# Kernel optimization log

Measured on AMD Instinct MI355X. Metric: run time of the kernel, lower is better.

The kernel has to match this reference:

```python
import jax, jax.numpy as jnp
import numpy as np
from jax import lax

H_IMG, W_IMG = 1280, 1280
STRIDES = (8, 16, 32, 64, 128)
FEAT_SHAPES = tuple((H_IMG // s) * (W_IMG // s) for s in STRIDES)  # (25600,6400,1600,400,100)
N_POINTS = sum(FEAT_SHAPES)  # 34100
NUM_CLASSES = 1
TOPK = 1000
SCORE_THRESH = 0.05
NMS_THRESH = 0.5
MAX_DET = 300
BATCH = 8
N_GT = 200


def make_points():
    # matches AnchorFreePS.reference_points: cell centers at stride*i + stride//2, (cx, cy) order
    pts = []
    for s in STRIDES:
        h, w = H_IMG // s, W_IMG // s
        cx = np.arange(w, dtype=np.float32) * s + s // 2
        cy = np.arange(h, dtype=np.float32) * s + s // 2
        gy, gx = np.meshgrid(cy, cx, indexing='ij')
        pts.append(np.stack([gx, gy], axis=-1).reshape(-1, 2))
    return jnp.asarray(np.concatenate(pts, axis=0))


def setup_inputs() -> dict:
    key = jax.random.key(0)
    k1, k2, k3, k4 = jax.random.split(key, 4)
    points = make_points()  # [N,2]
    xy = jax.random.uniform(k1, (BATCH, N_GT, 2), minval=0.0, maxval=1000.0)
    wh = jax.random.uniform(k2, (BATCH, N_GT, 2), minval=20.0, maxval=260.0)
    gt_boxes = jnp.concatenate([xy, xy + wh], axis=-1)  # [B,M,4] x1y1x2y2
    cls_logits = jax.random.normal(k3, (BATCH, N_POINTS, NUM_CLASSES)) * 1.5 - 3.0
    regression = jax.random.uniform(k4, (BATCH, N_POINTS, 4)) * 0.1  # normalized ltrb codes
    return {"points": points, "gt_boxes": gt_boxes, "cls_logits": cls_logits, "regression": regression}


def match_points_to_boxes(points, gt_boxes):
    # point-in-box test + area-cost argmin (compute_loss matched_idxs)
    px = points[None, :, None, 0]  # [1,N,1]
    py = points[None, :, None, 1]
    b = gt_boxes[:, None, :, :]    # [B,1,M,4]
    inside = (px >= b[..., 0]) & (px <= b[..., 2]) & (py >= b[..., 1]) & (py <= b[..., 3])  # [B,N,M]
    matched = jnp.any(inside, axis=-1)  # [B,N]
    areas = (gt_boxes[..., 2] - gt_boxes[..., 0]) * (gt_boxes[..., 3] - gt_boxes[..., 1])  # [B,M]
    BIG = jnp.float32(2 ** 31 - 1)  # torch.iinfo(torch.int).max
    cost = jnp.where(inside, areas[:, None, :], BIG)
    idx = jnp.argmin(cost, axis=-1)
    return jnp.where(matched, idx, -1)


def decode_boxes(rel, pts):
    # FCOSBoxCoder.decode_single with weights (1,1,1,1)
    l = rel[:, 0] * W_IMG
    t = rel[:, 1] * H_IMG
    r = rel[:, 2] * W_IMG
    b = rel[:, 3] * H_IMG
    x, y = pts[:, 0], pts[:, 1]
    return jnp.stack([x - l, y - t, x + r, y + b], axis=-1)


def clip_boxes(boxes):
    return jnp.stack([
        jnp.clip(boxes[:, 0], 0.0, W_IMG),
        jnp.clip(boxes[:, 1], 0.0, H_IMG),
        jnp.clip(boxes[:, 2], 0.0, W_IMG),
        jnp.clip(boxes[:, 3], 0.0, H_IMG)], axis=-1)


def nms(boxes, scores, labels, valid_init):
    # fixed-size sequential NMS equivalent to batched_nms (same-label suppression)
    work = lax.stop_gradient(jnp.where(valid_init, scores, -jnp.inf))

    def body(w, _):
        i = jnp.argmax(w)
        s = w[i]
        box = boxes[i]
        x1 = jnp.maximum(box[0], boxes[:, 0])
        y1 = jnp.maximum(box[1], boxes[:, 1])
        x2 = jnp.minimum(box[2], boxes[:, 2])
        y2 = jnp.minimum(box[3], boxes[:, 3])
        inter = jnp.clip(x2 - x1, 0.0) * jnp.clip(y2 - y1, 0.0)
        a1 = (box[2] - box[0]) * (box[3] - box[1])
        a2 = (boxes[:, 2] - boxes[:, 0]) * (boxes[:, 3] - boxes[:, 1])
        iou = inter / (a1 + a2 - inter + 1e-9)
        supp = (iou > NMS_THRESH) & (labels == labels[i])
        w = jnp.where(supp, -jnp.inf, w).at[i].set(-jnp.inf)
        return w, (i, s)

    _, (idxs, picked) = lax.scan(body, work, None, length=MAX_DET)
    valid = picked > -jnp.inf
    return idxs, valid


def postprocess_image(points, cls_i, reg_i):
    bx_list, sc_list, lb_list = [], [], []
    off = 0
    for size in FEAT_SHAPES:  # fixed small level loop
        sl = slice(off, off + size)
        off += size
        scores = jax.nn.sigmoid(cls_i[sl]).reshape(-1)  # [size*C]
        k = min(TOPK, size * NUM_CLASSES)
        sc, idx = lax.top_k(scores, k)
        a = idx // NUM_CLASSES
        lb = idx % NUM_CLASSES
        bx = clip_boxes(decode_boxes(reg_i[sl][a], points[sl][a]))
        bx_list.append(bx)
        sc_list.append(sc)
        lb_list.append(lb)
    boxes = jnp.concatenate(bx_list, axis=0)
    scores = jnp.concatenate(sc_list, axis=0)
    labels = jnp.concatenate(lb_list, axis=0)
    idxs, valid = nms(boxes, scores, labels, scores > SCORE_THRESH)
    out_boxes = jnp.where(valid[:, None], boxes[idxs], 0.0)
    out_scores = jnp.where(valid, scores[idxs], 0.0)
    out_labels = jnp.where(valid, labels[idxs], -1)
    return out_boxes, out_scores, out_labels, valid


def reference(points, gt_boxes, cls_logits, regression):
    matched_idxs = match_points_to_boxes(points, gt_boxes)  # [B,N]
    boxes, scores, labels, valid = jax.vmap(
        lambda c, r: postprocess_image(points, c, r))(cls_logits, regression)
    return matched_idxs, boxes, scores, labels, valid
```

## Files before the change

### kernel.cpp

```cpp
#include <hip/hip_runtime.h>
#include <stdint.h>

#define N_POINTS   34100
#define BATCH      8
#define N_GT       200
#define NLEV       5
#define NCAND      3500
#define MAX_DET    300
#define SCORE_TH   0.05f
#define NMS_TH     0.5f
#define IMG        1280.0f
#define NBIN       4096
#define TIE_CAP    4096
#define MTH 0.50000002980232238769531250

#define OUT_MATCH  0
#define OUT_BOXES  272800
#define OUT_SCORES 282400
#define OUT_LABELS 284800
#define OUT_VALID  287200

#define WS_KEYS    0
#define WS_SBOX    2632192
#define WS_SSC     3080192
#define WS_MASK    3192192
#define WS_DIAG    9500032
#define WS_HIST    WS_MASK
#define HSUB       8
#define MASK_STRIDE 98560
#define DIAG_STRIDE 3520


typedef unsigned long long u64;
typedef uint32_t u32;

__device__ __forceinline__ int mask_off(int c) {
    int g = c >> 6;
    return 64 * (55 * g - (g * (g - 1)) / 2) + (c - (g << 6)) * (55 - g);
}

__device__ __forceinline__ int level_of(int p) {
    return (p < 25600) ? 0 : (p < 32000) ? 1 : (p < 33600) ? 2 : (p < 34000) ? 3 : 4;
}
__device__ __forceinline__ int loff_of(int l) {
    return (l == 0) ? 0 : (l == 1) ? 25600 : (l == 2) ? 32000 : (l == 3) ? 33600 : 34000;
}
__device__ __forceinline__ int k_of(int l) {
    return (l == 0) ? 1000 : (l == 1) ? 1000 : (l == 2) ? 1000 : (l == 3) ? 400 : 100;
}
__device__ __forceinline__ u64 readlane64(u64 v, int t) {
    u32 lo = (u32)__builtin_amdgcn_readlane((int)(u32)v, t);
    u32 hi = (u32)__builtin_amdgcn_readlane((int)(u32)(v >> 32), t);
    return ((u64)hi << 32) | lo;
}

__global__ __launch_bounds__(1024)
void match_hist_kernel(const float* __restrict__ points,
                       const float* __restrict__ gt,
                       const float* __restrict__ logits,
                       float* __restrict__ out_match,
                       u32* __restrict__ keys,
                       u32* __restrict__ ghist) {
#pragma clang fp contract(off)
    __shared__ float bx1[N_GT], by1[N_GT], bx2[N_GT], by2[N_GT], ar[N_GT];
    __shared__ u32 hh[NBIN];
    const int b = blockIdx.x & 7;
    const int g = blockIdx.x >> 3;
    const int tid = threadIdx.x;

    if (g < 17) {
        const int base = g * 2048 + tid;
        for (int j = tid; j < N_GT; j += 1024) {
            float x1 = gt[(b * N_GT + j) * 4 + 0];
            float y1 = gt[(b * N_GT + j) * 4 + 1];
            float x2 = gt[(b * N_GT + j) * 4 + 2];
            float y2 = gt[(b * N_GT + j) * 4 + 3];
            bx1[j] = x1; by1[j] = y1; bx2[j] = x2; by2[j] = y2;
            ar[j] = (x2 - x1) * (y2 - y1);
        }
        __syncthreads();

        const float BIGF = 2147483648.0f;
        float px[2], py[2], best[2];
        int bi[2];
#pragma unroll
        for (int k = 0; k < 2; ++k) {
            int p = base + k * 1024;
            int pc = (p < N_POINTS) ? p : 0;
            px[k] = points[pc * 2 + 0];
            py[k] = points[pc * 2 + 1];
            best[k] = BIGF; bi[k] = -1;
        }
        for (int j = 0; j < N_GT; ++j) {
            float x1 = bx1[j], y1 = by1[j], x2 = bx2[j], y2 = by2[j], a = ar[j];
#pragma unroll
            for (int k = 0; k < 2; ++k) {
                bool inside = (px[k] >= x1) && (px[k] <= x2) &&
                              (py[k] >= y1) && (py[k] <= y2);
                float cost = inside ? a : BIGF;
                if (cost < best[k]) { best[k] = cost; bi[k] = j; }
            }
        }
#pragma unroll
        for (int k = 0; k < 2; ++k) {
            int p = base + k * 1024;
            if (p >= N_POINTS) continue;
            out_match[b * N_POINTS + p] = (float)bi[k];
        }
    } else {
        const int f = g - 17;
        int lev, sub, p0, cnt;
        if (f < 8)       { lev = 0; sub = f;     p0 = f * 3200;               cnt = 3200; }
        else if (f < 10) { lev = 1; sub = f - 8; p0 = 25600 + (f - 8) * 3200; cnt = 3200; }
        else if (f == 10){ lev = 2; sub = 0;     p0 = 32000;                  cnt = 1600; }
        else if (f == 11){ lev = 3; sub = 0;     p0 = 33600;                  cnt = 400;  }
        else             { lev = 4; sub = 0;     p0 = 34000;                  cnt = 100;  }

        for (int i = tid; i < NBIN; i += 1024) hh[i] = 0u;
        __syncthreads();

        for (int i = tid; i < cnt; i += 1024) {
            int p = p0 + i;
            float lg = logits[b * N_POINTS + p];
            float s = 1.0f / (1.0f + expf(-lg));
            u32 u = __float_as_uint(s);
            u32 key = (u & 0x80000000u) ? ~u : (u | 0x80000000u);
            keys[b * N_POINTS + p] = key;
            atomicAdd(&hh[(key >> 19) & 4095u], 1u);
        }
        __syncthreads();

        u32* outp = ghist + (((u32)b * NLEV + (u32)lev) * HSUB + (u32)sub) * NBIN;
        for (int i = tid; i < NBIN; i += 1024) outp[i] = hh[i];
    }
}

#define SORT_T 1024
#define LSWZ(j) (((j) & 63) * 65 + ((j) >> 6))
__global__ __launch_bounds__(SORT_T)
void pipeline_kernel(const u32* __restrict__ keys,
                     const u32* __restrict__ ghist,
                     const float* __restrict__ reg,
                     const float* __restrict__ points,
                     float* __restrict__ sboxes,
                     float* __restrict__ sscores) {
#pragma clang fp contract(off)
    __shared__ __align__(16) char smem[131072];
    u64* sk   = (u64*)smem;
    u64* tb   = (u64*)(smem + 32768);
    u64* aux  = (u64*)(smem + 65536);
    u32* h    = (u32*)(smem + 98304);
    u32* bs   = (u32*)(smem + 114688);
    u32* lsb  = (u32*)smem;
    __shared__ u32 sTl[NLEV], skkl[NLEV], wt[16];
    __shared__ u32 scnt, stcnt;

    const int b = blockIdx.x;
    const int tid = threadIdx.x;
    const int lane = tid & 63;
    const int wid = tid >> 6;
    const u32* kk_ = keys + b * N_POINTS;

    if (tid == 0) { scnt = 0u; stcnt = 0u; }

    {
        const u32* hb = ghist + (u32)b * (NLEV * HSUB * NBIN);
#pragma unroll
        for (int lev = 0; lev < NLEV; ++lev) {
            const int SUBS = (lev == 0) ? 8 : (lev == 1) ? 2 : 1;
            const u32* hl = hb + lev * HSUB * NBIN + tid;
            u32 s0 = 0, s1 = 0, s2 = 0, s3 = 0;
#pragma unroll
            for (int sub = 0; sub < SUBS; ++sub) {
                const u32* hs = hl + sub * NBIN;
                s0 += hs[0]; s1 += hs[1024]; s2 += hs[2048]; s3 += hs[3072];
            }
            u32* lv = lsb + lev * 4160;
            lv[LSWZ(tid)]        = s0;
            lv[LSWZ(tid + 1024)] = s1;
            lv[LSWZ(tid + 2048)] = s2;
            lv[LSWZ(tid + 3072)] = s3;
        }
        const uint4* kp4 = (const uint4*)kk_;
        u32 a0 = 0, a1 = 0, a2 = 0, a3 = 0;
        int i = tid;
        for (; i + 3072 < 8525; i += 4096) {
            uint4 v0 = kp4[i];
            uint4 v1 = kp4[i + 1024];
            uint4 v2 = kp4[i + 2048];
            uint4 v3 = kp4[i + 3072];
            a0 ^= v0.x ^ v0.y ^ v0.z ^ v0.w;
            a1 ^= v1.x ^ v1.y ^ v1.z ^ v1.w;
            a2 ^= v2.x ^ v2.y ^ v2.z ^ v2.w;
            a3 ^= v3.x ^ v3.y ^ v3.z ^ v3.w;
        }
        for (; i < 8525; i += 1024) {
            uint4 v = kp4[i];
            a0 ^= v.x ^ v.y ^ v.z ^ v.w;
        }
        u32 wacc = a0 ^ a1 ^ a2 ^ a3;
        asm volatile("" :: "v"(wacc));
    }
    __syncthreads();

    if (wid < NLEV) {
        const u32 K = (u32)k_of(wid);
        const u32* hh = lsb + wid * 4160;
        u32 S = 0;
#pragma unroll 16
        for (int i = 0; i < 64; ++i) S += hh[i * 65 + lane];
        u32 acc = S;
#pragma unroll
        for (int off = 1; off < 64; off <<= 1) {
            u32 v = (u32)__shfl_down((int)acc, off);
            if (lane + off < 64) acc += v;
        }
        u32 sfxAfter = acc - S;
        bool hit = (sfxAfter < K) && (sfxAfter + S >= K);
        u64 bal = __ballot(hit);
        int Lg = (int)__builtin_ctzll(bal);
        u32 sfxG = (u32)__shfl((int)sfxAfter, Lg);

        u32 v = hh[lane * 65 + Lg];
        u32 acc2 = v;
#pragma unroll
        for (int off = 1; off < 64; off <<= 1) {
            u32 t = (u32)__shfl_down((int)acc2, off);
            if (lane + off < 64) acc2 += t;
        }
        u32 sfx2 = sfxG + acc2 - v;
        bool hit2 = (sfx2 < K) && (sfx2 + v >= K);
        if (hit2) { sTl[wid] = (u32)(Lg * 64 + lane); skkl[wid] = K - sfx2; }
    }
    __syncthreads();

    const u64 below = (lane == 0) ? 0ull : (~0ull >> (64 - lane));
    const int CHUNK = 4 * SORT_T;
    for (int it = 0; it < (N_POINTS + CHUNK - 1) / CHUNK; ++it) {
        u32 key4[4]; int pc4[4]; bool act4[4];
#pragma unroll
        for (int u = 0; u < 4; ++u) {
            int i = it * CHUNK + u * SORT_T + tid;
            act4[u] = (i < N_POINTS);
            pc4[u] = act4[u] ? i : (N_POINTS - 1);
            key4[u] = kk_[pc4[u]];
        }
#pragma unroll
        for (int u = 0; u < 4; ++u) {
            bool active = act4[u];
            int pc = pc4[u];
            u32 key = key4[u];
            int l = level_of(pc);
            u32 digit = (key >> 19) & 4095u;
            u32 T = sTl[l];
            bool isDef = active && (digit > T);
            bool isTie = active && (digit == T);
            u64 k50 = ((u64)key << 18) | ((u64)(7 - l) << 15)
                    | (u64)(32767 - (pc - loff_of(l)));
            u64 grp = __ballot(isDef);
            if (grp) {
                int leader = (int)__builtin_ctzll(grp);
                u32 base_ = 0;
                if (lane == leader)
                    base_ = atomicAdd(&scnt, (u32)__builtin_popcountll(grp));
                base_ = (u32)__shfl((int)base_, leader);
                if (isDef) sk[base_ + (u32)__builtin_popcountll(grp & below)] = k50;
            }
            u64 tg = __ballot(isTie);
            if (tg) {
                int leader = (int)__builtin_ctzll(tg);
                u32 base_ = 0;
                if (lane == leader)
                    base_ = atomicAdd(&stcnt, (u32)__builtin_popcountll(tg));
                base_ = (u32)__shfl((int)base_, leader);
                if (isTie) {
                    u32 pos = base_ + (u32)__builtin_popcountll(tg & below);
                    if (pos < TIE_CAP) tb[pos] = k50;
                }
            }
        }
    }
    __syncthreads();

    int t = (int)stcnt; if (t > TIE_CAP) t = TIE_CAP;
    for (int j0 = tid; j0 - tid < t; j0 += SORT_T) {
        bool active = j0 < t;
        u64 kj = active ? tb[j0] : 0ull;
        u32 lvtag = (u32)(kj >> 15) & 7u;
        int r = 0;
        for (int i = 0; i < t; ++i) {
            u64 ki = tb[i];
            r += (ki > kj && (((u32)(ki >> 15) & 7u) == lvtag)) ? 1 : 0;
        }
        bool inc = active && (r < (int)skkl[7 - lvtag]);
        u64 grp = __ballot(inc);
        if (grp) {
            int leader = (int)__builtin_ctzll(grp);
            u32 base_ = 0;
            if (lane == leader)
                base_ = atomicAdd(&scnt, (u32)__builtin_popcountll(grp));
            base_ = (u32)__shfl((int)base_, leader);
            if (inc) sk[base_ + (u32)__builtin_popcountll(grp & below)] = kj;
        }
    }
    __syncthreads();
    const int total = (int)scnt;

    for (int i = tid; i < NBIN; i += SORT_T) h[i] = 0u;
    __syncthreads();
    for (int i = tid; i < total; i += SORT_T)
        atomicAdd(&h[(u32)(sk[i] >> 37) & 4095u], 1u);
    __syncthreads();

    u32 t0 = h[4095 - 4 * tid];
    u32 t1 = h[4095 - (4 * tid + 1)];
    u32 t2 = h[4095 - (4 * tid + 2)];
    u32 t3 = h[4095 - (4 * tid + 3)];
    u32 tsum = t0 + t1 + t2 + t3;
    u32 sc_ = tsum;
#pragma unroll
    for (int off = 1; off < 64; off <<= 1) {
        u32 v = (u32)__shfl_up((int)sc_, off);
        if (lane >= off) sc_ += v;
    }
    if (lane == 63) wt[wid] = sc_;
    __syncthreads();
    if (tid < 64) {
        u32 v = (tid < 16) ? wt[tid] : 0u;
        u32 s2 = v;
#pragma unroll
        for (int off = 1; off < 16; off <<= 1) {
            u32 x = (u32)__shfl_up((int)s2, off);
            if (tid >= off) s2 += x;
        }
        if (tid < 16) wt[tid] = s2 - v;
    }
    __syncthreads();
    u32 run = (sc_ - tsum) + wt[wid];
    bs[4095 - 4 * tid] = run;       run += t0;
    bs[4095 - (4 * tid + 1)] = run; run += t1;
    bs[4095 - (4 * tid + 2)] = run; run += t2;
    bs[4095 - (4 * tid + 3)] = run;
    __syncthreads();
    for (int i = tid; i < NBIN; i += SORT_T) h[i] = 0u;
    __syncthreads();
    for (int i = tid; i < total; i += SORT_T) {
        u64 k = sk[i];
        u32 d = (u32)(k >> 37) & 4095u;
        u32 pos = bs[d] + atomicAdd(&h[d], 1u);
        aux[pos] = k;
    }
    __syncthreads();
    for (int p = tid; p < total; p += SORT_T) {
        u64 kp = aux[p];
        u32 d = (u32)(kp >> 37) & 4095u;
        u32 gbase = bs[d];
        u32 gend = (d == 0) ? (u32)total : bs[d - 1];
        u32 r = 0;
        for (u32 q = gbase; q < gend; ++q) r += (aux[q] > kp) ? 1u : 0u;
        sk[gbase + r] = kp;
    }
    __syncthreads();

    for (int r = tid; r < NCAND; r += SORT_T) {
        float x1 = 0.f, y1 = 0.f, x2 = 0.f, y2 = 0.f, sc = 0.f;
        if (r < total) {
            u64 k50 = sk[r];
            int lowb = (int)(k50 & 0x3FFFFull);
            int l = 7 - (lowb >> 15);
            int idxl = 32767 - (lowb & 32767);
            int p = loff_of(l) + idxl;
            u32 key32 = (u32)(k50 >> 18);
            sc = __uint_as_float(key32 ^ 0x80000000u);
            int gp = b * N_POINTS + p;
            float l_ = reg[gp * 4 + 0] * IMG;
            float t_ = reg[gp * 4 + 1] * IMG;
            float r_ = reg[gp * 4 + 2] * IMG;
            float bb = reg[gp * 4 + 3] * IMG;
            float px = points[p * 2 + 0];
            float py = points[p * 2 + 1];
            x1 = fminf(fmaxf(px - l_, 0.0f), IMG);
            y1 = fminf(fmaxf(py - t_, 0.0f), IMG);
            x2 = fminf(fmaxf(px + r_, 0.0f), IMG);
            y2 = fminf(fmaxf(py + bb, 0.0f), IMG);
        }
        int slot = b * NCAND + r;
        sboxes[slot * 4 + 0] = x1;
        sboxes[slot * 4 + 1] = y1;
        sboxes[slot * 4 + 2] = x2;
        sboxes[slot * 4 + 3] = y2;
        sscores[slot] = sc;
    }
}

__global__ __launch_bounds__(256)
void mask_kernel(const float* __restrict__ sboxes,
                 const float* __restrict__ sscores,
                 u64* __restrict__ mask,
                 u64* __restrict__ diag) {
#pragma clang fp contract(off)
    const int b = blockIdx.x & 7;
    const int gx = blockIdx.x >> 3;
    const int wv = threadIdx.x >> 6;
    const int lane = threadIdx.x & 63;
    const int NG = (NCAND + 3) >> 2;
    const int NH = (NG + 1) >> 1;
    const int gidx = gx * 4 + wv;
    if (gidx >= NH) return;

    const float4* gb = (const float4*)sboxes + b * NCAND;
    const float* gs = sscores + b * NCAND;
    u64* mout = mask + (size_t)b * MASK_STRIDE;
    u64* dout = diag + (size_t)b * DIAG_STRIDE;

    for (int s = 0; s < 2; ++s) {
        const int g0 = (s == 0) ? gidx : (NG - 1 - gidx);
        if (s == 1 && g0 == gidx) break;
        const int c0 = g0 << 2;

        float4 bc[4]; float a1[4]; bool ok[4]; int g[4]; u64* rp[4];
        bool any = false;
#pragma unroll
        for (int i = 0; i < 4; ++i) {
            int c = c0 + i;
            int cc = (c < NCAND) ? c : (NCAND - 1);
            bc[i] = gb[cc];
            a1[i] = (bc[i].z - bc[i].x) * (bc[i].w - bc[i].y);
            ok[i] = (c < NCAND) && (gs[cc] > SCORE_TH);
            g[i] = cc >> 6;
            rp[i] = mout + mask_off(cc) - g[i];
            any |= ok[i];
        }
        if (!any) continue;

        for (int w = (c0 >> 6); w < 55; ++w) {
            int cj = (w << 6) + lane;
            float4 bj = (cj < NCAND) ? gb[cj] : make_float4(0.f, 0.f, 0.f, 0.f);
            float a2 = (bj.z - bj.x) * (bj.w - bj.y);
#pragma unroll
            for (int i = 0; i < 4; ++i) {
                float x1 = fmaxf(bc[i].x, bj.x);
                float y1 = fmaxf(bc[i].y, bj.y);
                float x2 = fminf(bc[i].z, bj.z);
                float y2 = fminf(bc[i].w, bj.w);
                float inter = fmaxf(x2 - x1, 0.f) * fmaxf(y2 - y1, 0.f);
                float denom = a1[i] + a2 - inter + 1e-9f;
                float hf = 0.5f * denom;
                float rr = fmaf(0x1p-25f, denom, hf);
                u64 bits = __ballot(inter > rr);
                u64 eq = __ballot(inter == rr);
                if (eq) {
                    u64 fb = __ballot((double)inter > MTH * (double)denom);
                    bits |= (eq & fb);
                }
                if (lane == 0 && ok[i] && w >= g[i]) {
                    rp[i][w] = bits;
                    if (w == g[i]) dout[c0 + i] = bits;
                }
            }
        }
    }
}

__global__ __launch_bounds__(1024)
void scan_kernel(const float* __restrict__ sboxes,
                 const float* __restrict__ sscores,
                 const u64* __restrict__ mask,
                 const u64* __restrict__ diag,
                 float* __restrict__ out) {
    __shared__ u32 pick_idx[MAX_DET];
    const int b = blockIdx.x;
    const int tid = threadIdx.x;
    const u64* mrow = mask + (size_t)b * MASK_STRIDE;
    const u64* drow = diag + (size_t)b * DIAG_STRIDE;
    const float4* gb = (const float4*)sboxes + b * NCAND;
    const float* gs = sscores + b * NCAND;

    if (tid >= 64) {
        const uint4* mp = (const uint4*)mrow;
        const uint4* dp = (const uint4*)drow;
        const uint4* bp = (const uint4*)gb;
        const uint4* sp = (const uint4*)gs;
        const int t = tid - 64;
        u32 a0 = 0, a1 = 0, a2 = 0, a3 = 0, a4 = 0, a5 = 0, a6 = 0, a7 = 0;
        int i = t;
        for (; i + 6720 < 49280; i += 7680) {
            uint4 v0 = mp[i];
            uint4 v1 = mp[i + 960];
            uint4 v2 = mp[i + 1920];
            uint4 v3 = mp[i + 2880];
            uint4 v4 = mp[i + 3840];
            uint4 v5 = mp[i + 4800];
            uint4 v6 = mp[i + 5760];
            uint4 v7 = mp[i + 6720];
            a0 ^= v0.x ^ v0.y ^ v0.z ^ v0.w;
            a1 ^= v1.x ^ v1.y ^ v1.z ^ v1.w;
            a2 ^= v2.x ^ v2.y ^ v2.z ^ v2.w;
            a3 ^= v3.x ^ v3.y ^ v3.z ^ v3.w;
            a4 ^= v4.x ^ v4.y ^ v4.z ^ v4.w;
            a5 ^= v5.x ^ v5.y ^ v5.z ^ v5.w;
            a6 ^= v6.x ^ v6.y ^ v6.z ^ v6.w;
            a7 ^= v7.x ^ v7.y ^ v7.z ^ v7.w;
        }
        for (; i < 49280; i += 960) {
            uint4 v = mp[i];
            a0 ^= v.x ^ v.y ^ v.z ^ v.w;
        }
        if (t < 880) {
            uint4 v0 = dp[t];
            uint4 v1 = dp[t + 880];
            a1 ^= v0.x ^ v0.y ^ v0.z ^ v0.w;
            a2 ^= v1.x ^ v1.y ^ v1.z ^ v1.w;
        }
        for (int j = t; j < 3500; j += 960) {
            uint4 v = bp[j];
            a3 ^= v.x ^ v.y ^ v.z ^ v.w;
        }
        if (t < 875) {
            uint4 v = sp[t];
            a4 ^= v.x ^ v.y ^ v.z ^ v.w;
        }
        u32 acc = (a0 ^ a1) ^ (a2 ^ a3) ^ (a4 ^ a5) ^ (a6 ^ a7);
        asm volatile("" :: "v"(acc));
        return;
    }

    const int lane = tid;

    float* ob = out + OUT_BOXES  + b * MAX_DET * 4;
    float* os = out + OUT_SCORES + b * MAX_DET;
    float* ol = out + OUT_LABELS + b * MAX_DET;
    float* ov = out + OUT_VALID  + b * MAX_DET;

    u64 m = 0ull;
    u64 rowN = drow[lane];
    float sjN = gs[lane];

    int kept = 0;
    for (int w = 0; w < 55; ++w) {
        const int wbase = w << 6;
        const u64 row = rowN;
        const float sj = sjN;
        if (w < 54) {
            int cn = wbase + 64 + lane;
            int cc = (cn < NCAND) ? cn : (NCAND - 1);
            rowN = drow[cc];
            float s = gs[cc];
            sjN = (cn < NCAND) ? s : 0.f;
        }
        int c = wbase + lane;
        u64 bad = __ballot(!((c < NCAND) && (sj > SCORE_TH)));
        u64 cur = readlane64(m, w) | bad;
        u64 km = 0ull;
        while (kept < MAX_DET) {
            u64 avail = ~cur;
            if (avail == 0ull) break;
            int t = (int)__builtin_ctzll(avail);
            u64 r = readlane64(row, t);
            cur |= r | (1ull << t);
            km |= 1ull << t;
            if (lane == 0) pick_idx[kept] = (u32)(wbase + t);
            kept++;
        }
        if (km) {
            const bool lr = (lane >= w && lane < 55);
            const int lo = lane - w;
            u64 acc = 0ull;
            while (km) {
#define POPBIT(tn) int tn = -1; if (km) { tn = (int)__builtin_ctzll(km); km &= km - 1ull; }
                POPBIT(t0) POPBIT(t1) POPBIT(t2) POPBIT(t3)
                POPBIT(t4) POPBIT(t5) POPBIT(t6) POPBIT(t7)
#undef POPBIT
                u64 v0 = 0, v1 = 0, v2 = 0, v3 = 0, v4 = 0, v5 = 0, v6 = 0, v7 = 0;
                if (lr) {
                    v0 = mrow[mask_off(wbase + t0) + lo];
                    if (t1 >= 0) v1 = mrow[mask_off(wbase + t1) + lo];
                    if (t2 >= 0) v2 = mrow[mask_off(wbase + t2) + lo];
                    if (t3 >= 0) v3 = mrow[mask_off(wbase + t3) + lo];
                    if (t4 >= 0) v4 = mrow[mask_off(wbase + t4) + lo];
                    if (t5 >= 0) v5 = mrow[mask_off(wbase + t5) + lo];
                    if (t6 >= 0) v6 = mrow[mask_off(wbase + t6) + lo];
                    if (t7 >= 0) v7 = mrow[mask_off(wbase + t7) + lo];
                }
                acc |= ((v0 | v1) | (v2 | v3)) | ((v4 | v5) | (v6 | v7));
            }
            m |= acc;
        }
        if (kept >= MAX_DET) break;
    }

    for (int k = lane; k < kept; k += 64) {
        u32 c = pick_idx[k];
        float4 bx = gb[c];
        float s = gs[c];
        ob[k * 4 + 0] = bx.x;
        ob[k * 4 + 1] = bx.y;
        ob[k * 4 + 2] = bx.z;
        ob[k * 4 + 3] = bx.w;
        os[k] = s;
        ol[k] = 0.0f;
        ov[k] = 1.0f;
    }
    for (int k = kept + lane; k < MAX_DET; k += 64) {
        ob[k * 4 + 0] = 0.f; ob[k * 4 + 1] = 0.f;
        ob[k * 4 + 2] = 0.f; ob[k * 4 + 3] = 0.f;
        os[k] = 0.f; ol[k] = -1.f; ov[k] = 0.f;
    }
}

extern "C" void kernel_launch(void* const* d_in, const int* in_sizes, int n_in,
                              void* d_out, int out_size, void* d_ws, size_t ws_size,
                              hipStream_t stream) {
    const float* points = (const float*)d_in[0];
    const float* gt     = (const float*)d_in[1];
    const float* logits = (const float*)d_in[2];
    const float* reg    = (const float*)d_in[3];
    float* out = (float*)d_out;

    u32* keys      = (u32*)((char*)d_ws + WS_KEYS);
    float* sboxes  = (float*)((char*)d_ws + WS_SBOX);
    float* sscores = (float*)((char*)d_ws + WS_SSC);
    u64* mask   = (u64*)((char*)d_ws + WS_MASK);
    u64* diag   = (u64*)((char*)d_ws + WS_DIAG);
    u32* ghist  = (u32*)((char*)d_ws + WS_HIST);

    match_hist_kernel<<<30 * BATCH, 1024, 0, stream>>>(points, gt, logits,
                                                       out + OUT_MATCH, keys, ghist);

    pipeline_kernel<<<BATCH, SORT_T, 0, stream>>>(keys, ghist, reg, points,
                                                  sboxes, sscores);

    mask_kernel<<<110 * BATCH, 256, 0, stream>>>(sboxes, sscores, mask, diag);

    scan_kernel<<<BATCH, 1024, 0, stream>>>(sboxes, sscores, mask, diag, out);
}
```

Before: 228.2 us.

## Fuse four kernels into one cooperative persistent kernel with grid syncs

```diff
diff --git a/kernel.cpp b/kernel.cpp
--- a/kernel.cpp
+++ b/kernel.cpp
@@ -1,5 +1,8 @@
 #include <hip/hip_runtime.h>
+#include <hip/hip_cooperative_groups.h>
 #include <stdint.h>
+
+namespace cg = cooperative_groups;
 
 #define N_POINTS   34100
 #define BATCH      8
@@ -38,7 +41,6 @@
     int g = c >> 6;
     return 64 * (55 * g - (g * (g - 1)) / 2) + (c - (g << 6)) * (55 - g);
 }
-
 __device__ __forceinline__ int level_of(int p) {
     return (p < 25600) ? 0 : (p < 32000) ? 1 : (p < 33600) ? 2 : (p < 34000) ? 3 : 4;
 }
@@ -54,61 +56,35 @@
     return ((u64)hi << 32) | lo;
 }
 
+#define LSWZ(j) (((j) & 63) * 65 + ((j) >> 6))
+
 __global__ __launch_bounds__(1024)
-void match_hist_kernel(const float* __restrict__ points,
-                       const float* __restrict__ gt,
-                       const float* __restrict__ logits,
-                       float* __restrict__ out_match,
-                       u32* __restrict__ keys,
-                       u32* __restrict__ ghist) {
+void mega_kernel(const float* __restrict__ points,
+                 const float* __restrict__ gt,
+                 const float* __restrict__ logits,
+                 const float* __restrict__ reg,
+                 float* __restrict__ out,
+                 u32* __restrict__ keys,
+                 float* __restrict__ sboxes,
+                 float* __restrict__ sscores,
+                 u64* __restrict__ maskg,
+                 u64* __restrict__ diag,
+                 u32* __restrict__ ghist) {
 #pragma clang fp contract(off)
-    __shared__ float bx1[N_GT], by1[N_GT], bx2[N_GT], by2[N_GT], ar[N_GT];
-    __shared__ u32 hh[NBIN];
-    const int b = blockIdx.x & 7;
-    const int g = blockIdx.x >> 3;
+    cg::grid_group grid = cg::this_grid();
+    __shared__ __align__(16) char smem[131072];
+    __shared__ u32 sTl[NLEV], skkl[NLEV], wt[16];
+    __shared__ u32 scnt, stcnt;
+
+    const int bid = blockIdx.x;
     const int tid = threadIdx.x;
-
-    if (g < 17) {
-        const int base = g * 2048 + tid;
-        for (int j = tid; j < N_GT; j += 1024) {
-            float x1 = gt[(b * N_GT + j) * 4 + 0];
-            float y1 = gt[(b * N_GT + j) * 4 + 1];
-            float x2 = gt[(b * N_GT + j) * 4 + 2];
-            float y2 = gt[(b * N_GT + j) * 4 + 3];
-            bx1[j] = x1; by1[j] = y1; bx2[j] = x2; by2[j] = y2;
-            ar[j] = (x2 - x1) * (y2 - y1);
-        }
-        __syncthreads();
-
-        const float BIGF = 2147483648.0f;
-        float px[2], py[2], best[2];
-        int bi[2];
-#pragma unroll
-        for (int k = 0; k < 2; ++k) {
-            int p = base + k * 1024;
-            int pc = (p < N_POINTS) ? p : 0;
-            px[k] = points[pc * 2 + 0];
-            py[k] = points[pc * 2 + 1];
-            best[k] = BIGF; bi[k] = -1;
-        }
-        for (int j = 0; j < N_GT; ++j) {
-            float x1 = bx1[j], y1 = by1[j], x2 = bx2[j], y2 = by2[j], a = ar[j];
-#pragma unroll
-            for (int k = 0; k < 2; ++k) {
-                bool inside = (px[k] >= x1) && (px[k] <= x2) &&
-                              (py[k] >= y1) && (py[k] <= y2);
-                float cost = inside ? a : BIGF;
-                if (cost < best[k]) { best[k] = cost; bi[k] = j; }
-            }
-        }
-#pragma unroll
-        for (int k = 0; k < 2; ++k) {
-            int p = base + k * 1024;
-            if (p >= N_POINTS) continue;
-            out_match[b * N_POINTS + p] = (float)bi[k];
-        }
-    } else {
-        const int f = g - 17;
+    const int lane = tid & 63;
+    const int wid = tid >> 6;
+
+    if (bid < 104) {
+        u32* hh = (u32*)smem;
+        const int b = bid & 7;
+        const int f = bid >> 3;
         int lev, sub, p0, cnt;
         if (f < 8)       { lev = 0; sub = f;     p0 = f * 3200;               cnt = 3200; }
         else if (f < 10) { lev = 1; sub = f - 8; p0 = 25600 + (f - 8) * 3200; cnt = 3200; }
@@ -118,7 +94,6 @@
 
         for (int i = tid; i < NBIN; i += 1024) hh[i] = 0u;
         __syncthreads();
-
         for (int i = tid; i < cnt; i += 1024) {
             int p = p0 + i;
             float lg = logits[b * N_POINTS + p];
@@ -129,482 +104,502 @@
             atomicAdd(&hh[(key >> 19) & 4095u], 1u);
         }
         __syncthreads();
-
         u32* outp = ghist + (((u32)b * NLEV + (u32)lev) * HSUB + (u32)sub) * NBIN;
         for (int i = tid; i < NBIN; i += 1024) outp[i] = hh[i];
     }
-}
-
-#define SORT_T 1024
-#define LSWZ(j) (((j) & 63) * 65 + ((j) >> 6))
-__global__ __launch_bounds__(SORT_T)
-void pipeline_kernel(const u32* __restrict__ keys,
-                     const u32* __restrict__ ghist,
-                     const float* __restrict__ reg,
-                     const float* __restrict__ points,
-                     float* __restrict__ sboxes,
-                     float* __restrict__ sscores) {
-#pragma clang fp contract(off)
-    __shared__ __align__(16) char smem[131072];
-    u64* sk   = (u64*)smem;
-    u64* tb   = (u64*)(smem + 32768);
-    u64* aux  = (u64*)(smem + 65536);
-    u32* h    = (u32*)(smem + 98304);
-    u32* bs   = (u32*)(smem + 114688);
-    u32* lsb  = (u32*)smem;
-    __shared__ u32 sTl[NLEV], skkl[NLEV], wt[16];
-    __shared__ u32 scnt, stcnt;
-
-    const int b = blockIdx.x;
-    const int tid = threadIdx.x;
-    const int lane = tid & 63;
-    const int wid = tid >> 6;
-    const u32* kk_ = keys + b * N_POINTS;
-
-    if (tid == 0) { scnt = 0u; stcnt = 0u; }
-
-    {
-        const u32* hb = ghist + (u32)b * (NLEV * HSUB * NBIN);
-#pragma unroll
-        for (int lev = 0; lev < NLEV; ++lev) {
-            const int SUBS = (lev == 0) ? 8 : (lev == 1) ? 2 : 1;
-            const u32* hl = hb + lev * HSUB * NBIN + tid;
-            u32 s0 = 0, s1 = 0, s2 = 0, s3 = 0;
-#pragma unroll
-            for (int sub = 0; sub < SUBS; ++sub) {
-                const u32* hs = hl + sub * NBIN;
-                s0 += hs[0]; s1 += hs[1024]; s2 += hs[2048]; s3 += hs[3072];
-            }
-            u32* lv = lsb + lev * 4160;
-            lv[LSWZ(tid)]        = s0;
-            lv[LSWZ(tid + 1024)] = s1;
-            lv[LSWZ(tid + 2048)] = s2;
-            lv[LSWZ(tid + 3072)] = s3;
-        }
-        const uint4* kp4 = (const uint4*)kk_;
-        u32 a0 = 0, a1 = 0, a2 = 0, a3 = 0;
-        int i = tid;
-        for (; i + 3072 < 8525; i += 4096) {
-            uint4 v0 = kp4[i];
-            uint4 v1 = kp4[i + 1024];
-            uint4 v2 = kp4[i + 2048];
-            uint4 v3 = kp4[i + 3072];
-            a0 ^= v0.x ^ v0.y ^ v0.z ^ v0.w;
-            a1 ^= v1.x ^ v1.y ^ v1.z ^ v1.w;
-            a2 ^= v2.x ^ v2.y ^ v2.z ^ v2.w;
-            a3 ^= v3.x ^ v3.y ^ v3.z ^ v3.w;
-        }
-        for (; i < 8525; i += 1024) {
-            uint4 v = kp4[i];
-            a0 ^= v.x ^ v.y ^ v.z ^ v.w;
-        }
-        u32 wacc = a0 ^ a1 ^ a2 ^ a3;
-        asm volatile("" :: "v"(wacc));
-    }
-    __syncthreads();
-
-    if (wid < NLEV) {
-        const u32 K = (u32)k_of(wid);
-        const u32* hh = lsb + wid * 4160;
-        u32 S = 0;
+    __threadfence();
+    grid.sync();
+
+    if (bid < 8) {
+        u64* sk   = (u64*)smem;
+        u64* tb   = (u64*)(smem + 32768);
+        u64* aux  = (u64*)(smem + 65536);
+        u32* h    = (u32*)(smem + 98304);
+        u32* bs   = (u32*)(smem + 114688);
+        u32* lsb  = (u32*)smem;
+        const int b = bid;
+        const u32* kk_ = keys + b * N_POINTS;
+
+        if (tid == 0) { scnt = 0u; stcnt = 0u; }
+
+        {
+            const u32* hb = ghist + (u32)b * (NLEV * HSUB * NBIN);
+#pragma unroll
+            for (int lev = 0; lev < NLEV; ++lev) {
+                const int SUBS = (lev == 0) ? 8 : (lev == 1) ? 2 : 1;
+                const u32* hl = hb + lev * HSUB * NBIN + tid;
+                u32 s0 = 0, s1 = 0, s2 = 0, s3 = 0;
+#pragma unroll
+                for (int sub = 0; sub < SUBS; ++sub) {
+                    const u32* hs = hl + sub * NBIN;
+                    s0 += hs[0]; s1 += hs[1024]; s2 += hs[2048]; s3 += hs[3072];
+                }
+                u32* lv = lsb + lev * 4160;
+                lv[LSWZ(tid)]        = s0;
+                lv[LSWZ(tid + 1024)] = s1;
+                lv[LSWZ(tid + 2048)] = s2;
+                lv[LSWZ(tid + 3072)] = s3;
+            }
+            const uint4* kp4 = (const uint4*)kk_;
+            u32 a0 = 0, a1 = 0, a2 = 0, a3 = 0;
+            int i = tid;
+            for (; i + 3072 < 8525; i += 4096) {
+                uint4 v0 = kp4[i];
+                uint4 v1 = kp4[i + 1024];
+                uint4 v2 = kp4[i + 2048];
+                uint4 v3 = kp4[i + 3072];
+                a0 ^= v0.x ^ v0.y ^ v0.z ^ v0.w;
+                a1 ^= v1.x ^ v1.y ^ v1.z ^ v1.w;
+                a2 ^= v2.x ^ v2.y ^ v2.z ^ v2.w;
+                a3 ^= v3.x ^ v3.y ^ v3.z ^ v3.w;
+            }
+            for (; i < 8525; i += 1024) {
+                uint4 v = kp4[i];
+                a0 ^= v.x ^ v.y ^ v.z ^ v.w;
+            }
+            u32 wacc = a0 ^ a1 ^ a2 ^ a3;
+            asm volatile("" :: "v"(wacc));
+        }
+        __syncthreads();
+
+        if (wid < NLEV) {
+            const u32 K = (u32)k_of(wid);
+            const u32* hh2 = lsb + wid * 4160;
+            u32 S = 0;
 #pragma unroll 16
-        for (int i = 0; i < 64; ++i) S += hh[i * 65 + lane];
-        u32 acc = S;
-#pragma unroll
-        for (int off = 1; off < 64; off <<= 1) {
-            u32 v = (u32)__shfl_down((int)acc, off);
-            if (lane + off < 64) acc += v;
-        }
-        u32 sfxAfter = acc - S;
-        bool hit = (sfxAfter < K) && (sfxAfter + S >= K);
-        u64 bal = __ballot(hit);
-        int Lg = (int)__builtin_ctzll(bal);
-        u32 sfxG = (u32)__shfl((int)sfxAfter, Lg);
-
-        u32 v = hh[lane * 65 + Lg];
-        u32 acc2 = v;
-#pragma unroll
-        for (int off = 1; off < 64; off <<= 1) {
-            u32 t = (u32)__shfl_down((int)acc2, off);
-            if (lane + off < 64) acc2 += t;
-        }
-        u32 sfx2 = sfxG + acc2 - v;
-        bool hit2 = (sfx2 < K) && (sfx2 + v >= K);
-        if (hit2) { sTl[wid] = (u32)(Lg * 64 + lane); skkl[wid] = K - sfx2; }
-    }
-    __syncthreads();
-
-    const u64 below = (lane == 0) ? 0ull : (~0ull >> (64 - lane));
-    const int CHUNK = 4 * SORT_T;
-    for (int it = 0; it < (N_POINTS + CHUNK - 1) / CHUNK; ++it) {
-        u32 key4[4]; int pc4[4]; bool act4[4];
-#pragma unroll
-        for (int u = 0; u < 4; ++u) {
-            int i = it * CHUNK + u * SORT_T + tid;
-            act4[u] = (i < N_POINTS);
-            pc4[u] = act4[u] ? i : (N_POINTS - 1);
-            key4[u] = kk_[pc4[u]];
-        }
-#pragma unroll
-        for (int u = 0; u < 4; ++u) {
-            bool active = act4[u];
-            int pc = pc4[u];
-            u32 key = key4[u];
-            int l = level_of(pc);
-            u32 digit = (key >> 19) & 4095u;
-            u32 T = sTl[l];
-            bool isDef = active && (digit > T);
-            bool isTie = active && (digit == T);
-            u64 k50 = ((u64)key << 18) | ((u64)(7 - l) << 15)
-                    | (u64)(32767 - (pc - loff_of(l)));
-            u64 grp = __ballot(isDef);
+            for (int i = 0; i < 64; ++i) S += hh2[i * 65 + lane];
+            u32 acc = S;
+#pragma unroll
+            for (int off = 1; off < 64; off <<= 1) {
+                u32 v = (u32)__shfl_down((int)acc, off);
+                if (lane + off < 64) acc += v;
+            }
+            u32 sfxAfter = acc - S;
+            bool hit = (sfxAfter < K) && (sfxAfter + S >= K);
+            u64 bal = __ballot(hit);
+            int Lg = (int)__builtin_ctzll(bal);
+            u32 sfxG = (u32)__shfl((int)sfxAfter, Lg);
+
+            u32 v = hh2[lane * 65 + Lg];
+            u32 acc2 = v;
+#pragma unroll
+            for (int off = 1; off < 64; off <<= 1) {
+                u32 t = (u32)__shfl_down((int)acc2, off);
+                if (lane + off < 64) acc2 += t;
+            }
+            u32 sfx2 = sfxG + acc2 - v;
+            bool hit2 = (sfx2 < K) && (sfx2 + v >= K);
+            if (hit2) { sTl[wid] = (u32)(Lg * 64 + lane); skkl[wid] = K - sfx2; }
+        }
+        __syncthreads();
+
+        const u64 below = (lane == 0) ? 0ull : (~0ull >> (64 - lane));
+        const int CHUNK = 4 * 1024;
+        for (int it = 0; it < (N_POINTS + CHUNK - 1) / CHUNK; ++it) {
+            u32 key4[4]; int pc4[4]; bool act4[4];
+#pragma unroll
+            for (int u = 0; u < 4; ++u) {
+                int i = it * CHUNK + u * 1024 + tid;
+                act4[u] = (i < N_POINTS);
+                pc4[u] = act4[u] ? i : (N_POINTS - 1);
+                key4[u] = kk_[pc4[u]];
+            }
+#pragma unroll
+            for (int u = 0; u < 4; ++u) {
+                bool active = act4[u];
+                int pc = pc4[u];
+                u32 key = key4[u];
+                int l = level_of(pc);
+                u32 digit = (key >> 19) & 4095u;
+                u32 T = sTl[l];
+                bool isDef = active && (digit > T);
+                bool isTie = active && (digit == T);
+                u64 k50 = ((u64)key << 18) | ((u64)(7 - l) << 15)
+                        | (u64)(32767 - (pc - loff_of(l)));
+                u64 grp = __ballot(isDef);
+                if (grp) {
+                    int leader = (int)__builtin_ctzll(grp);
+                    u32 base_ = 0;
+                    if (lane == leader)
+                        base_ = atomicAdd(&scnt, (u32)__builtin_popcountll(grp));
+                    base_ = (u32)__shfl((int)base_, leader);
+                    if (isDef) sk[base_ + (u32)__builtin_popcountll(grp & below)] = k50;
+                }
+                u64 tg = __ballot(isTie);
+                if (tg) {
+                    int leader = (int)__builtin_ctzll(tg);
+                    u32 base_ = 0;
+                    if (lane == leader)
+                        base_ = atomicAdd(&stcnt, (u32)__builtin_popcountll(tg));
+                    base_ = (u32)__shfl((int)base_, leader);
+                    if (isTie) {
+                        u32 pos = base_ + (u32)__builtin_popcountll(tg & below);
+                        if (pos < TIE_CAP) tb[pos] = k50;
+                    }
+                }
+            }
+        }
+        __syncthreads();
+
+        int t = (int)stcnt; if (t > TIE_CAP) t = TIE_CAP;
+        for (int j0 = tid; j0 - tid < t; j0 += 1024) {
+            bool active = j0 < t;
+            u64 kj = active ? tb[j0] : 0ull;
+            u32 lvtag = (u32)(kj >> 15) & 7u;
+            int r = 0;
+            for (int i = 0; i < t; ++i) {
+                u64 ki = tb[i];
+                r += (ki > kj && (((u32)(ki >> 15) & 7u) == lvtag)) ? 1 : 0;
+            }
+            bool inc = active && (r < (int)skkl[7 - lvtag]);
+            u64 grp = __ballot(inc);
             if (grp) {
                 int leader = (int)__builtin_ctzll(grp);
                 u32 base_ = 0;
                 if (lane == leader)
                     base_ = atomicAdd(&scnt, (u32)__builtin_popcountll(grp));
                 base_ = (u32)__shfl((int)base_, leader);
-                if (isDef) sk[base_ + (u32)__builtin_popcountll(grp & below)] = k50;
-            }
-            u64 tg = __ballot(isTie);
-            if (tg) {
-                int leader = (int)__builtin_ctzll(tg);
-                u32 base_ = 0;
-                if (lane == leader)
-                    base_ = atomicAdd(&stcnt, (u32)__builtin_popcountll(tg));
-                base_ = (u32)__shfl((int)base_, leader);
-                if (isTie) {
-                    u32 pos = base_ + (u32)__builtin_popcountll(tg & below);
-                    if (pos < TIE_CAP) tb[pos] = k50;
+                if (inc) sk[base_ + (u32)__builtin_popcountll(grp & below)] = kj;
+            }
+        }
+        __syncthreads();
+        const int total = (int)scnt;
+
+        for (int i = tid; i < NBIN; i += 1024) h[i] = 0u;
+        __syncthreads();
+        for (int i = tid; i < total; i += 1024)
+            atomicAdd(&h[(u32)(sk[i] >> 37) & 4095u], 1u);
+        __syncthreads();
+
+        u32 t0 = h[4095 - 4 * tid];
+        u32 t1 = h[4095 - (4 * tid + 1)];
+        u32 t2 = h[4095 - (4 * tid + 2)];
+        u32 t3 = h[4095 - (4 * tid + 3)];
+        u32 tsum = t0 + t1 + t2 + t3;
+        u32 sc_ = tsum;
+#pragma unroll
+        for (int off = 1; off < 64; off <<= 1) {
+            u32 v = (u32)__shfl_up((int)sc_, off);
+            if (lane >= off) sc_ += v;
+        }
+        if (lane == 63) wt[wid] = sc_;
+        __syncthreads();
+        if (tid < 64) {
+            u32 v = (tid < 16) ? wt[tid] : 0u;
+            u32 s2 = v;
+#pragma unroll
+            for (int off = 1; off < 16; off <<= 1) {
+                u32 x = (u32)__shfl_up((int)s2, off);
+                if (tid >= off) s2 += x;
+            }
+            if (tid < 16) wt[tid] = s2 - v;
+        }
+        __syncthreads();
+        u32 run = (sc_ - tsum) + wt[wid];
+        bs[4095 - 4 * tid] = run;       run += t0;
+        bs[4095 - (4 * tid + 1)] = run; run += t1;
+        bs[4095 - (4 * tid + 2)] = run; run += t2;
+        bs[4095 - (4 * tid + 3)] = run;
+        __syncthreads();
+        for (int i = tid; i < NBIN; i += 1024) h[i] = 0u;
+        __syncthreads();
+        for (int i = tid; i < total; i += 1024) {
+            u64 k = sk[i];
+            u32 d = (u32)(k >> 37) & 4095u;
+            u32 pos = bs[d] + atomicAdd(&h[d], 1u);
+            aux[pos] = k;
+        }
+        __syncthreads();
+        for (int p = tid; p < total; p += 1024) {
+            u64 kp = aux[p];
+            u32 d = (u32)(kp >> 37) & 4095u;
+            u32 gbase = bs[d];
+            u32 gend = (d == 0) ? (u32)total : bs[d - 1];
+            u32 r = 0;
+            for (u32 q = gbase; q < gend; ++q) r += (aux[q] > kp) ? 1u : 0u;
+            sk[gbase + r] = kp;
+        }
+        __syncthreads();
+
+        for (int r = tid; r < NCAND; r += 1024) {
+            float x1 = 0.f, y1 = 0.f, x2 = 0.f, y2 = 0.f, sc = 0.f;
+            if (r < total) {
+                u64 k50 = sk[r];
+                int lowb = (int)(k50 & 0x3FFFFull);
+                int l = 7 - (lowb >> 15);
+                int idxl = 32767 - (lowb & 32767);
+                int p = loff_of(l) + idxl;
+                u32 key32 = (u32)(k50 >> 18);
+                sc = __uint_as_float(key32 ^ 0x80000000u);
+                int gp = b * N_POINTS + p;
+                float l_ = reg[gp * 4 + 0] * IMG;
+                float t_ = reg[gp * 4 + 1] * IMG;
+                float r_ = reg[gp * 4 + 2] * IMG;
+                float bb = reg[gp * 4 + 3] * IMG;
+                float px = points[p * 2 + 0];
+                float py = points[p * 2 + 1];
+                x1 = fminf(fmaxf(px - l_, 0.0f), IMG);
+                y1 = fminf(fmaxf(py - t_, 0.0f), IMG);
+                x2 = fminf(fmaxf(px + r_, 0.0f), IMG);
+                y2 = fminf(fmaxf(py + bb, 0.0f), IMG);
+            }
+            int slot = b * NCAND + r;
+            sboxes[slot * 4 + 0] = x1;
+            sboxes[slot * 4 + 1] = y1;
+            sboxes[slot * 4 + 2] = x2;
+            sboxes[slot * 4 + 3] = y2;
+            sscores[slot] = sc;
+        }
+    } else if (bid < 144) {
+        float* bx1 = (float*)smem;
+        float* by1 = (float*)(smem + 1024);
+        float* bx2 = (float*)(smem + 2048);
+        float* by2 = (float*)(smem + 3072);
+        float* ar  = (float*)(smem + 4096);
+        const int mt = bid - 8;
+        const int b = mt & 7;
+        const int g = mt >> 3;
+        const int base = g * 2048 + tid;
+
+        for (int j = tid; j < N_GT; j += 1024) {
+            float x1 = gt[(b * N_GT + j) * 4 + 0];
+            float y1 = gt[(b * N_GT + j) * 4 + 1];
+            float x2 = gt[(b * N_GT + j) * 4 + 2];
+            float y2 = gt[(b * N_GT + j) * 4 + 3];
+            bx1[j] = x1; by1[j] = y1; bx2[j] = x2; by2[j] = y2;
+            ar[j] = (x2 - x1) * (y2 - y1);
+        }
+        __syncthreads();
+
+        const float BIGF = 2147483648.0f;
+        float px[2], py[2], best[2];
+        int bi[2];
+#pragma unroll
+        for (int k = 0; k < 2; ++k) {
+            int p = base + k * 1024;
+            int pc = (p < N_POINTS) ? p : 0;
+            px[k] = points[pc * 2 + 0];
+            py[k] = points[pc * 2 + 1];
+            best[k] = BIGF; bi[k] = -1;
+        }
+        for (int j = 0; j < N_GT; ++j) {
+            float x1 = bx1[j], y1 = by1[j], x2 = bx2[j], y2 = by2[j], a = ar[j];
+#pragma unroll
+            for (int k = 0; k < 2; ++k) {
+                bool inside = (px[k] >= x1) && (px[k] <= x2) &&
+                              (py[k] >= y1) && (py[k] <= y2);
+                float cost = inside ? a : BIGF;
+                if (cost < best[k]) { best[k] = cost; bi[k] = j; }
+            }
+        }
+#pragma unroll
+        for (int k = 0; k < 2; ++k) {
+            int p = base + k * 1024;
+            if (p < N_POINTS) out[OUT_MATCH + b * N_POINTS + p] = (float)bi[k];
+        }
+    }
+    __threadfence();
+    grid.sync();
+
+    {
+        const int b = bid & 7;
+        const int NG = (NCAND + 3) >> 2;
+        const int NH = (NG + 1) >> 1;
+        const int gidx = (bid >> 3) * 16 + wid;
+        if (gidx < NH) {
+            const float4* gb = (const float4*)sboxes + b * NCAND;
+            const float* gs = sscores + b * NCAND;
+            u64* mout = maskg + (size_t)b * MASK_STRIDE;
+            u64* dout = diag + (size_t)b * DIAG_STRIDE;
+
+            for (int s = 0; s < 2; ++s) {
+                const int g0 = (s == 0) ? gidx : (NG - 1 - gidx);
+                if (s == 1 && g0 == gidx) break;
+                const int c0 = g0 << 2;
+
+                float4 bc[4]; float a1[4]; bool ok[4]; int g[4]; u64* rp[4];
+                bool any = false;
+#pragma unroll
+                for (int i = 0; i < 4; ++i) {
+                    int c = c0 + i;
+                    int cc = (c < NCAND) ? c : (NCAND - 1);
+                    bc[i] = gb[cc];
+                    a1[i] = (bc[i].z - bc[i].x) * (bc[i].w - bc[i].y);
+                    ok[i] = (c < NCAND) && (gs[cc] > SCORE_TH);
+                    g[i] = cc >> 6;
+                    rp[i] = mout + mask_off(cc) - g[i];
+                    any |= ok[i];
                 }
+                if (!any) continue;
+
+                for (int w = (c0 >> 6); w < 55; ++w) {
+                    int cj = (w << 6) + lane;
+                    float4 bj = (cj < NCAND) ? gb[cj] : make_float4(0.f, 0.f, 0.f, 0.f);
+                    float a2 = (bj.z - bj.x) * (bj.w - bj.y);
+#pragma unroll
+                    for (int i = 0; i < 4; ++i) {
+                        float x1 = fmaxf(bc[i].x, bj.x);
+                        float y1 = fmaxf(bc[i].y, bj.y);
+                        float x2 = fminf(bc[i].z, bj.z);
+                        float y2 = fminf(bc[i].w, bj.w);
+                        float inter = fmaxf(x2 - x1, 0.f) * fmaxf(y2 - y1, 0.f);
+                        float denom = a1[i] + a2 - inter + 1e-9f;
+                        float hf = 0.5f * denom;
+                        float rr = fmaf(0x1p-25f, denom, hf);
+                        u64 bits = __ballot(inter > rr);
+                        u64 eq = __ballot(inter == rr);
+                        if (eq) {
+                            u64 fb = __ballot((double)inter > MTH * (double)denom);
+                            bits |= (eq & fb);
+                        }
+                        if (lane == 0 && ok[i] && w >= g[i]) {
+                            rp[i][w] = bits;
+                            if (w == g[i]) dout[c0 + i] = bits;
+                        }
+                    }
+                }
             }
         }
     }
-    __syncthreads();
-
-    int t = (int)stcnt; if (t > TIE_CAP) t = TIE_CAP;
-    for (int j0 = tid; j0 - tid < t; j0 += SORT_T) {
-        bool active = j0 < t;
-        u64 kj = active ? tb[j0] : 0ull;
-        u32 lvtag = (u32)(kj >> 15) & 7u;
-        int r = 0;
-        for (int i = 0; i < t; ++i) {
-            u64 ki = tb[i];
-            r += (ki > kj && (((u32)(ki >> 15) & 7u) == lvtag)) ? 1 : 0;
-        }
-        bool inc = active && (r < (int)skkl[7 - lvtag]);
-        u64 grp = __ballot(inc);
-        if (grp) {
-            int leader = (int)__builtin_ctzll(grp);
-            u32 base_ = 0;
-            if (lane == leader)
-                base_ = atomicAdd(&scnt, (u32)__builtin_popcountll(grp));
-            base_ = (u32)__shfl((int)base_, leader);
-            if (inc) sk[base_ + (u32)__builtin_popcountll(grp & below)] = kj;
-        }
-    }
-    __syncthreads();
-    const int total = (int)scnt;
-
-    for (int i = tid; i < NBIN; i += SORT_T) h[i] = 0u;
-    __syncthreads();
-    for (int i = tid; i < total; i += SORT_T)
-        atomicAdd(&h[(u32)(sk[i] >> 37) & 4095u], 1u);
-    __syncthreads();
-
-    u32 t0 = h[4095 - 4 * tid];
-    u32 t1 = h[4095 - (4 * tid + 1)];
-    u32 t2 = h[4095 - (4 * tid + 2)];
-    u32 t3 = h[4095 - (4 * tid + 3)];
-    u32 tsum = t0 + t1 + t2 + t3;
-    u32 sc_ = tsum;
-#pragma unroll
-    for (int off = 1; off < 64; off <<= 1) {
-        u32 v = (u32)__shfl_up((int)sc_, off);
-        if (lane >= off) sc_ += v;
-    }
-    if (lane == 63) wt[wid] = sc_;
-    __syncthreads();
-    if (tid < 64) {
-        u32 v = (tid < 16) ? wt[tid] : 0u;
-        u32 s2 = v;
-#pragma unroll
-        for (int off = 1; off < 16; off <<= 1) {
-            u32 x = (u32)__shfl_up((int)s2, off);
-            if (tid >= off) s2 += x;
-        }
-        if (tid < 16) wt[tid] = s2 - v;
-    }
-    __syncthreads();
-    u32 run = (sc_ - tsum) + wt[wid];
-    bs[4095 - 4 * tid] = run;       run += t0;
-    bs[4095 - (4 * tid + 1)] = run; run += t1;
-    bs[4095 - (4 * tid + 2)] = run; run += t2;
-    bs[4095 - (4 * tid + 3)] = run;
-    __syncthreads();
-    for (int i = tid; i < NBIN; i += SORT_T) h[i] = 0u;
-    __syncthreads();
-    for (int i = tid; i < total; i += SORT_T) {
-        u64 k = sk[i];
-        u32 d = (u32)(k >> 37) & 4095u;
-        u32 pos = bs[d] + atomicAdd(&h[d], 1u);
-        aux[pos] = k;
-    }
-    __syncthreads();
-    for (int p = tid; p < total; p += SORT_T) {
-        u64 kp = aux[p];
-        u32 d = (u32)(kp >> 37) & 4095u;
-        u32 gbase = bs[d];
-        u32 gend = (d == 0) ? (u32)total : bs[d - 1];
-        u32 r = 0;
-        for (u32 q = gbase; q < gend; ++q) r += (aux[q] > kp) ? 1u : 0u;
-        sk[gbase + r] = kp;
-    }
-    __syncthreads();
-
-    for (int r = tid; r < NCAND; r += SORT_T) {
-        float x1 = 0.f, y1 = 0.f, x2 = 0.f, y2 = 0.f, sc = 0.f;
-        if (r < total) {
-            u64 k50 = sk[r];
-            int lowb = (int)(k50 & 0x3FFFFull);
-            int l = 7 - (lowb >> 15);
-            int idxl = 32767 - (lowb & 32767);
-            int p = loff_of(l) + idxl;
-            u32 key32 = (u32)(k50 >> 18);
-            sc = __uint_as_float(key32 ^ 0x80000000u);
-            int gp = b * N_POINTS + p;
-            float l_ = reg[gp * 4 + 0] * IMG;
-            float t_ = reg[gp * 4 + 1] * IMG;
-            float r_ = reg[gp * 4 + 2] * IMG;
-            float bb = reg[gp * 4 + 3] * IMG;
-            float px = points[p * 2 + 0];
-            float py = points[p * 2 + 1];
-            x1 = fminf(fmaxf(px - l_, 0.0f), IMG);
-            y1 = fminf(fmaxf(py - t_, 0.0f), IMG);
-            x2 = fminf(fmaxf(px + r_, 0.0f), IMG);
-            y2 = fminf(fmaxf(py + bb, 0.0f), IMG);
-        }
-        int slot = b * NCAND + r;
-        sboxes[slot * 4 + 0] = x1;
-        sboxes[slot * 4 + 1] = y1;
-        sboxes[slot * 4 + 2] = x2;
-        sboxes[slot * 4 + 3] = y2;
-        sscores[slot] = sc;
-    }
-}
-
-__global__ __launch_bounds__(256)
-void mask_kernel(const float* __restrict__ sboxes,
-                 const float* __restrict__ sscores,
-                 u64* __restrict__ mask,
-                 u64* __restrict__ diag) {
-#pragma clang fp contract(off)
-    const int b = blockIdx.x & 7;
-    const int gx = blockIdx.x >> 3;
-    const int wv = threadIdx.x >> 6;
-    const int lane = threadIdx.x & 63;
-    const int NG = (NCAND + 3) >> 2;
-    const int NH = (NG + 1) >> 1;
-    const int gidx = gx * 4 + wv;
-    if (gidx >= NH) return;
-
-    const float4* gb = (const float4*)sboxes + b * NCAND;
-    const float* gs = sscores + b * NCAND;
-    u64* mout = mask + (size_t)b * MASK_STRIDE;
-    u64* dout = diag + (size_t)b * DIAG_STRIDE;
-
-    for (int s = 0; s < 2; ++s) {
-        const int g0 = (s == 0) ? gidx : (NG - 1 - gidx);
-        if (s == 1 && g0 == gidx) break;
-        const int c0 = g0 << 2;
-
-        float4 bc[4]; float a1[4]; bool ok[4]; int g[4]; u64* rp[4];
-        bool any = false;
-#pragma unroll
-        for (int i = 0; i < 4; ++i) {
-            int c = c0 + i;
-            int cc = (c < NCAND) ? c : (NCAND - 1);
-            bc[i] = gb[cc];
-            a1[i] = (bc[i].z - bc[i].x) * (bc[i].w - bc[i].y);
-            ok[i] = (c < NCAND) && (gs[cc] > SCORE_TH);
-            g[i] = cc >> 6;
-            rp[i] = mout + mask_off(cc) - g[i];
-            any |= ok[i];
-        }
-        if (!any) continue;
-
-        for (int w = (c0 >> 6); w < 55; ++w) {
-            int cj = (w << 6) + lane;
-            float4 bj = (cj < NCAND) ? gb[cj] : make_float4(0.f, 0.f, 0.f, 0.f);
-            float a2 = (bj.z - bj.x) * (bj.w - bj.y);
-#pragma unroll
-            for (int i = 0; i < 4; ++i) {
-                float x1 = fmaxf(bc[i].x, bj.x);
-                float y1 = fmaxf(bc[i].y, bj.y);
-                float x2 = fminf(bc[i].z, bj.z);
-                float y2 = fminf(bc[i].w, bj.w);
-                float inter = fmaxf(x2 - x1, 0.f) * fmaxf(y2 - y1, 0.f);
-                float denom = a1[i] + a2 - inter + 1e-9f;
-                float hf = 0.5f * denom;
-                float rr = fmaf(0x1p-25f, denom, hf);
-                u64 bits = __ballot(inter > rr);
-                u64 eq = __ballot(inter == rr);
-                if (eq) {
-                    u64 fb = __ballot((double)inter > MTH * (double)denom);
-                    bits |= (eq & fb);
+    __threadfence();
+    grid.sync();
+
+    if (bid < 8) {
+        u32* pick_idx = (u32*)smem;
+        const int b = bid;
+        const u64* mrow = maskg + (size_t)b * MASK_STRIDE;
+        const u64* drow = diag + (size_t)b * DIAG_STRIDE;
+        const float4* gb = (const float4*)sboxes + b * NCAND;
+        const float* gs = sscores + b * NCAND;
+
+        if (tid >= 64) {
+            const uint4* mp = (const uint4*)mrow;
+            const uint4* dp = (const uint4*)drow;
+            const uint4* bp = (const uint4*)gb;
+            const uint4* sp = (const uint4*)gs;
+            const int t = tid - 64;
+            u32 a0 = 0, a1 = 0, a2 = 0, a3 = 0, a4 = 0, a5 = 0, a6 = 0, a7 = 0;
+            int i = t;
+            for (; i + 6720 < 49280; i += 7680) {
+                uint4 v0 = mp[i];
+                uint4 v1 = mp[i + 960];
+                uint4 v2 = mp[i + 1920];
+                uint4 v3 = mp[i + 2880];
+                uint4 v4 = mp[i + 3840];
+                uint4 v5 = mp[i + 4800];
+                uint4 v6 = mp[i + 5760];
+                uint4 v7 = mp[i + 6720];
+                a0 ^= v0.x ^ v0.y ^ v0.z ^ v0.w;
+                a1 ^= v1.x ^ v1.y ^ v1.z ^ v1.w;
+                a2 ^= v2.x ^ v2.y ^ v2.z ^ v2.w;
+                a3 ^= v3.x ^ v3.y ^ v3.z ^ v3.w;
+                a4 ^= v4.x ^ v4.y ^ v4.z ^ v4.w;
+                a5 ^= v5.x ^ v5.y ^ v5.z ^ v5.w;
+                a6 ^= v6.x ^ v6.y ^ v6.z ^ v6.w;
+                a7 ^= v7.x ^ v7.y ^ v7.z ^ v7.w;
+            }
+            for (; i < 49280; i += 960) {
+                uint4 v = mp[i];
+                a0 ^= v.x ^ v.y ^ v.z ^ v.w;
+            }
+            if (t < 880) {
+                uint4 v0 = dp[t];
+                uint4 v1 = dp[t + 880];
+                a1 ^= v0.x ^ v0.y ^ v0.z ^ v0.w;
+                a2 ^= v1.x ^ v1.y ^ v1.z ^ v1.w;
+            }
+            for (int j = t; j < 3500; j += 960) {
+                uint4 v = bp[j];
+                a3 ^= v.x ^ v.y ^ v.z ^ v.w;
+            }
+            if (t < 875) {
+                uint4 v = sp[t];
+                a4 ^= v.x ^ v.y ^ v.z ^ v.w;
+            }
+            u32 acc = (a0 ^ a1) ^ (a2 ^ a3) ^ (a4 ^ a5) ^ (a6 ^ a7);
+            asm volatile("" :: "v"(acc));
+            return;
+        }
+
+        float* ob = out + OUT_BOXES  + b * MAX_DET * 4;
+        float* os = out + OUT_SCORES + b * MAX_DET;
+        float* ol = out + OUT_LABELS + b * MAX_DET;
+        float* ov = out + OUT_VALID  + b * MAX_DET;
+
+        u64 m = 0ull;
+        u64 rowN = drow[lane];
+        float sjN = gs[lane];
+
+        int kept = 0;
+        for (int w = 0; w < 55; ++w) {
+            const int wbase = w << 6;
+            const u64 row = rowN;
+            const float sj = sjN;
+            if (w < 54) {
+                int cn = wbase + 64 + lane;
+                int cc = (cn < NCAND) ? cn : (NCAND - 1);
+                rowN = drow[cc];
+                float s = gs[cc];
+                sjN = (cn < NCAND) ? s : 0.f;
+            }
+            int c = wbase + lane;
+            u64 bad = __ballot(!((c < NCAND) && (sj > SCORE_TH)));
+            u64 cur = readlane64(m, w) | bad;
+            u64 km = 0ull;
+            while (kept < MAX_DET) {
+                u64 avail = ~cur;
+                if (avail == 0ull) break;
+                int t = (int)__builtin_ctzll(avail);
+                u64 r = readlane64(row, t);
+                cur |= r | (1ull << t);
+                km |= 1ull << t;
+                if (lane == 0) pick_idx[kept] = (u32)(wbase + t);
+                kept++;
+            }
+            if (km) {
+                const bool lr = (lane >= w && lane < 55);
+                const int lo = lane - w;
+                u64 acc = 0ull;
+                while (km) {
+#define POPBIT(tn) int tn = -1; if (km) { tn = (int)__builtin_ctzll(km); km &= km - 1ull; }
+                    POPBIT(t0) POPBIT(t1) POPBIT(t2) POPBIT(t3)
+                    POPBIT(t4) POPBIT(t5) POPBIT(t6) POPBIT(t7)
+#undef POPBIT
+                    u64 v0 = 0, v1 = 0, v2 = 0, v3 = 0, v4 = 0, v5 = 0, v6 = 0, v7 = 0;
+                    if (lr) {
+                        v0 = mrow[mask_off(wbase + t0) + lo];
+                        if (t1 >= 0) v1 = mrow[mask_off(wbase + t1) + lo];
+                        if (t2 >= 0) v2 = mrow[mask_off(wbase + t2) + lo];
+                        if (t3 >= 0) v3 = mrow[mask_off(wbase + t3) + lo];
+                        if (t4 >= 0) v4 = mrow[mask_off(wbase + t4) + lo];
+                        if (t5 >= 0) v5 = mrow[mask_off(wbase + t5) + lo];
+                        if (t6 >= 0) v6 = mrow[mask_off(wbase + t6) + lo];
+                        if (t7 >= 0) v7 = mrow[mask_off(wbase + t7) + lo];
+                    }
+                    acc |= ((v0 | v1) | (v2 | v3)) | ((v4 | v5) | (v6 | v7));
                 }
-                if (lane == 0 && ok[i] && w >= g[i]) {
-                    rp[i][w] = bits;
-                    if (w == g[i]) dout[c0 + i] = bits;
-                }
-            }
-        }
-    }
-}
-
-__global__ __launch_bounds__(1024)
-void scan_kernel(const float* __restrict__ sboxes,
-                 const float* __restrict__ sscores,
-                 const u64* __restrict__ mask,
-                 const u64* __restrict__ diag,
-                 float* __restrict__ out) {
-    __shared__ u32 pick_idx[MAX_DET];
-    const int b = blockIdx.x;
-    const int tid = threadIdx.x;
-    const u64* mrow = mask + (size_t)b * MASK_STRIDE;
-    const u64* drow = diag + (size_t)b * DIAG_STRIDE;
-    const float4* gb = (const float4*)sboxes + b * NCAND;
-    const float* gs = sscores + b * NCAND;
-
-    if (tid >= 64) {
-        const uint4* mp = (const uint4*)mrow;
-        const uint4* dp = (const uint4*)drow;
-        const uint4* bp = (const uint4*)gb;
-        const uint4* sp = (const uint4*)gs;
-        const int t = tid - 64;
-        u32 a0 = 0, a1 = 0, a2 = 0, a3 = 0, a4 = 0, a5 = 0, a6 = 0, a7 = 0;
-        int i = t;
-        for (; i + 6720 < 49280; i += 7680) {
-            uint4 v0 = mp[i];
-            uint4 v1 = mp[i + 960];
-            uint4 v2 = mp[i + 1920];
-            uint4 v3 = mp[i + 2880];
-            uint4 v4 = mp[i + 3840];
-            uint4 v5 = mp[i + 4800];
-            uint4 v6 = mp[i + 5760];
-            uint4 v7 = mp[i + 6720];
-            a0 ^= v0.x ^ v0.y ^ v0.z ^ v0.w;
-            a1 ^= v1.x ^ v1.y ^ v1.z ^ v1.w;
-            a2 ^= v2.x ^ v2.y ^ v2.z ^ v2.w;
-            a3 ^= v3.x ^ v3.y ^ v3.z ^ v3.w;
-            a4 ^= v4.x ^ v4.y ^ v4.z ^ v4.w;
-            a5 ^= v5.x ^ v5.y ^ v5.z ^ v5.w;
-            a6 ^= v6.x ^ v6.y ^ v6.z ^ v6.w;
-            a7 ^= v7.x ^ v7.y ^ v7.z ^ v7.w;
-        }
-        for (; i < 49280; i += 960) {
-            uint4 v = mp[i];
-            a0 ^= v.x ^ v.y ^ v.z ^ v.w;
-        }
-        if (t < 880) {
-            uint4 v0 = dp[t];
-            uint4 v1 = dp[t + 880];
-            a1 ^= v0.x ^ v0.y ^ v0.z ^ v0.w;
-            a2 ^= v1.x ^ v1.y ^ v1.z ^ v1.w;
-        }
-        for (int j = t; j < 3500; j += 960) {
-            uint4 v = bp[j];
-            a3 ^= v.x ^ v.y ^ v.z ^ v.w;
-        }
-        if (t < 875) {
-            uint4 v = sp[t];
-            a4 ^= v.x ^ v.y ^ v.z ^ v.w;
-        }
-        u32 acc = (a0 ^ a1) ^ (a2 ^ a3) ^ (a4 ^ a5) ^ (a6 ^ a7);
-        asm volatile("" :: "v"(acc));
-        return;
-    }
-
-    const int lane = tid;
-
-    float* ob = out + OUT_BOXES  + b * MAX_DET * 4;
-    float* os = out + OUT_SCORES + b * MAX_DET;
-    float* ol = out + OUT_LABELS + b * MAX_DET;
-    float* ov = out + OUT_VALID  + b * MAX_DET;
-
-    u64 m = 0ull;
-    u64 rowN = drow[lane];
-    float sjN = gs[lane];
-
-    int kept = 0;
-    for (int w = 0; w < 55; ++w) {
-        const int wbase = w << 6;
-        const u64 row = rowN;
-        const float sj = sjN;
-        if (w < 54) {
-            int cn = wbase + 64 + lane;
-            int cc = (cn < NCAND) ? cn : (NCAND - 1);
-            rowN = drow[cc];
-            float s = gs[cc];
-            sjN = (cn < NCAND) ? s : 0.f;
-        }
-        int c = wbase + lane;
-        u64 bad = __ballot(!((c < NCAND) && (sj > SCORE_TH)));
-        u64 cur = readlane64(m, w) | bad;
-        u64 km = 0ull;
-        while (kept < MAX_DET) {
-            u64 avail = ~cur;
-            if (avail == 0ull) break;
-            int t = (int)__builtin_ctzll(avail);
-            u64 r = readlane64(row, t);
-            cur |= r | (1ull << t);
-            km |= 1ull << t;
-            if (lane == 0) pick_idx[kept] = (u32)(wbase + t);
-            kept++;
-        }
-        if (km) {
-            const bool lr = (lane >= w && lane < 55);
-            const int lo = lane - w;
-            u64 acc = 0ull;
-            while (km) {
-#define POPBIT(tn) int tn = -1; if (km) { tn = (int)__builtin_ctzll(km); km &= km - 1ull; }
-                POPBIT(t0) POPBIT(t1) POPBIT(t2) POPBIT(t3)
-                POPBIT(t4) POPBIT(t5) POPBIT(t6) POPBIT(t7)
-#undef POPBIT
-                u64 v0 = 0, v1 = 0, v2 = 0, v3 = 0, v4 = 0, v5 = 0, v6 = 0, v7 = 0;
-                if (lr) {
-                    v0 = mrow[mask_off(wbase + t0) + lo];
-                    if (t1 >= 0) v1 = mrow[mask_off(wbase + t1) + lo];
-                    if (t2 >= 0) v2 = mrow[mask_off(wbase + t2) + lo];
-                    if (t3 >= 0) v3 = mrow[mask_off(wbase + t3) + lo];
-                    if (t4 >= 0) v4 = mrow[mask_off(wbase + t4) + lo];
-                    if (t5 >= 0) v5 = mrow[mask_off(wbase + t5) + lo];
-                    if (t6 >= 0) v6 = mrow[mask_off(wbase + t6) + lo];
-                    if (t7 >= 0) v7 = mrow[mask_off(wbase + t7) + lo];
-                }
-                acc |= ((v0 | v1) | (v2 | v3)) | ((v4 | v5) | (v6 | v7));
-            }
-            m |= acc;
-        }
-        if (kept >= MAX_DET) break;
-    }
-
-    for (int k = lane; k < kept; k += 64) {
-        u32 c = pick_idx[k];
-        float4 bx = gb[c];
-        float s = gs[c];
-        ob[k * 4 + 0] = bx.x;
-        ob[k * 4 + 1] = bx.y;
-        ob[k * 4 + 2] = bx.z;
-        ob[k * 4 + 3] = bx.w;
-        os[k] = s;
-        ol[k] = 0.0f;
-        ov[k] = 1.0f;
-    }
-    for (int k = kept + lane; k < MAX_DET; k += 64) {
-        ob[k * 4 + 0] = 0.f; ob[k * 4 + 1] = 0.f;
-        ob[k * 4 + 2] = 0.f; ob[k * 4 + 3] = 0.f;
-        os[k] = 0.f; ol[k] = -1.f; ov[k] = 0.f;
+                m |= acc;
+            }
+            if (kept >= MAX_DET) break;
+        }
+
+        for (int k = lane; k < kept; k += 64) {
+            u32 c = pick_idx[k];
+            float4 bx = gb[c];
+            float s = gs[c];
+            ob[k * 4 + 0] = bx.x;
+            ob[k * 4 + 1] = bx.y;
+            ob[k * 4 + 2] = bx.z;
+            ob[k * 4 + 3] = bx.w;
+            os[k] = s;
+            ol[k] = 0.0f;
+            ov[k] = 1.0f;
+        }
+        for (int k = kept + lane; k < MAX_DET; k += 64) {
+            ob[k * 4 + 0] = 0.f; ob[k * 4 + 1] = 0.f;
+            ob[k * 4 + 2] = 0.f; ob[k * 4 + 3] = 0.f;
+            os[k] = 0.f; ol[k] = -1.f; ov[k] = 0.f;
+        }
     }
 }
 
@@ -624,13 +619,9 @@
     u64* diag   = (u64*)((char*)d_ws + WS_DIAG);
     u32* ghist  = (u32*)((char*)d_ws + WS_HIST);
 
-    match_hist_kernel<<<30 * BATCH, 1024, 0, stream>>>(points, gt, logits,
-                                                       out + OUT_MATCH, keys, ghist);
-
-    pipeline_kernel<<<BATCH, SORT_T, 0, stream>>>(keys, ghist, reg, points,
-                                                  sboxes, sscores);
-
-    mask_kernel<<<110 * BATCH, 256, 0, stream>>>(sboxes, sscores, mask, diag);
-
-    scan_kernel<<<BATCH, 1024, 0, stream>>>(sboxes, sscores, mask, diag, out);
+    void* args[] = { (void*)&points, (void*)&gt, (void*)&logits, (void*)&reg,
+                     (void*)&out, (void*)&keys, (void*)&sboxes, (void*)&sscores,
+                     (void*)&mask, (void*)&diag, (void*)&ghist };
+    hipLaunchCooperativeKernel((const void*)mega_kernel, dim3(256), dim3(1024),
+                               args, 0, stream);
 }
```

New measurement: 525.0 us. 2.3x slower.
